# Kernel tuning notes

Measured on AMD Instinct MI355X. Metric: run time of the kernel, lower is better.

The kernel has to match this reference:

```python
import jax, jax.numpy as jnp
import numpy as np

DIM = 768
HEADS = 12
HEAD_DIM = DIM // HEADS
SCALE = HEAD_DIM ** -0.5


def setup_inputs() -> dict:
    key = jax.random.key(0)
    k1, k2, k3, k4, k5 = jax.random.split(key, 5)
    B, N = 4, 2048
    x = jax.random.normal(k1, (B, N, DIM), dtype=jnp.float32)
    # qkv Linear: weight [3*dim, dim], bias [3*dim]
    w_qkv = jax.random.normal(k2, (3 * DIM, DIM), dtype=jnp.float32) * (DIM ** -0.5)
    b_qkv = jax.random.normal(k3, (3 * DIM,), dtype=jnp.float32) * 0.01
    # proj Linear: weight [dim, dim], bias [dim]
    w_proj = jax.random.normal(k4, (DIM, DIM), dtype=jnp.float32) * (DIM ** -0.5)
    b_proj = jax.random.normal(k5, (DIM,), dtype=jnp.float32) * 0.01
    return {"x": x, "w_qkv": w_qkv, "b_qkv": b_qkv, "w_proj": w_proj, "b_proj": b_proj}


def reference(x, w_qkv, b_qkv, w_proj, b_proj):
    B, N, C = x.shape
    qkv = (jnp.einsum('bnc,oc->bno', x, w_qkv) + b_qkv)
    qkv = qkv.reshape(B, N, 3, HEADS, HEAD_DIM).transpose(2, 0, 3, 1, 4)
    q, k, v = qkv[0], qkv[1], qkv[2]
    attn = jnp.einsum('bhqd,bhkd->bhqk', q, k) * SCALE
    attn = jax.nn.softmax(attn, axis=-1)
    out = jnp.einsum('bhqk,bhkd->bhqd', attn, v)  # [B, H, N, Dh]
    out = out.transpose(0, 2, 1, 3).reshape(B, N, C)
    # dropout is identity in eval mode
    return jnp.einsum('bnc,oc->bno', out, w_proj) + b_proj
```

## Files before the change

### kernel.cpp

```cpp
#include <hip/hip_runtime.h>
#include <hip/hip_bf16.h>

using bf16 = __hip_bfloat16;
typedef __bf16 bf16x8 __attribute__((ext_vector_type(8)));
typedef short short4v __attribute__((ext_vector_type(4)));
typedef short short8v __attribute__((ext_vector_type(8)));
typedef float float4v __attribute__((ext_vector_type(4)));

#define DIM   768
#define NH    12
#define HD    64
#define SEQ   2048
#define BATCH 4
#define TOK   (BATCH * SEQ)
#define SCALE_QL2E 0.18033688011112042f

#define NX  (TOK * DIM)
#define NWQ (3 * DIM * DIM)
#define NWP (DIM * DIM)

__device__ __forceinline__ short f2bf(float f) {
  union { bf16 h; short s; } u;
  u.h = __float2bfloat16(f);
  return u.s;
}

union frag8 { short4v h[2]; short8v s; bf16x8 b; };

__device__ __forceinline__ void async_copy16(const bf16* g, short* l) {
  __builtin_amdgcn_global_load_lds(
      (const __attribute__((address_space(1))) unsigned int*)g,
      (__attribute__((address_space(3))) unsigned int*)l, 16, 0, 0);
}
__device__ __forceinline__ void async_copy4(const bf16* g, short* l) {
  __builtin_amdgcn_global_load_lds(
      (const __attribute__((address_space(1))) unsigned int*)g,
      (__attribute__((address_space(3))) unsigned int*)l, 4, 0, 0);
}

#define BARRIER __builtin_amdgcn_s_barrier()
#define LGKM0 asm volatile("s_waitcnt lgkmcnt(0)" ::: "memory")
#define VW0 asm volatile("s_waitcnt vmcnt(0)" ::: "memory")
#define NOSTG (void)0
#define NOVW  (void)0

__global__ void __launch_bounds__(256)
cvt3(const float* __restrict__ a, bf16* __restrict__ oa, long na,
     const float* __restrict__ b, bf16* __restrict__ ob, long nb,
     const float* __restrict__ c, bf16* __restrict__ oc, long nc) {
  const long i = ((long)blockIdx.x * 256 + threadIdx.x) * 8;
  const float* src; bf16* dst; long off;
  if (i < na)                { src = a; dst = oa; off = i; }
  else if (i < na + nb)      { src = b; dst = ob; off = i - na; }
  else if (i < na + nb + nc) { src = c; dst = oc; off = i - na - nb; }
  else return;
  const float4v x0 = *(const float4v*)(src + off);
  const float4v x1 = *(const float4v*)(src + off + 4);
  short8v r;
  r[0] = f2bf(x0[0]); r[1] = f2bf(x0[1]); r[2] = f2bf(x0[2]); r[3] = f2bf(x0[3]);
  r[4] = f2bf(x1[0]); r[5] = f2bf(x1[1]); r[6] = f2bf(x1[2]); r[7] = f2bf(x1[3]);
  *(short8v*)(dst + off) = r;
}

__device__ __forceinline__ void gemm_mainloop(const bf16* __restrict__ A,
                                              const bf16* __restrict__ B,
                                              short* As, short* Bs,
                                              float4v acc[4][4]) {
  const int t = threadIdx.x;
  const int w = t >> 6, l = t & 63, lr = l & 15, q = l >> 4;
  const int wr = ((w >> 1) << 6), wc = ((w & 1) << 6);

  const bf16* Ag = A + (t >> 2) * DIM + (t & 3) * 8;
  const bf16* Bg = B + (t >> 2) * DIM + (t & 3) * 8;

  for (int k0 = 0; k0 < DIM; k0 += 32) {
    __syncthreads();
    async_copy16(Ag,            &As[t * 8]);
    async_copy16(Ag + 64 * DIM, &As[2048 + t * 8]);
    async_copy16(Bg,            &Bs[t * 8]);
    async_copy16(Bg + 64 * DIM, &Bs[2048 + t * 8]);
    Ag += 32; Bg += 32;
    __syncthreads();

    bf16x8 af[4], bfv[4];
#pragma unroll
    for (int i = 0; i < 4; ++i)
      af[i] = *(const bf16x8*)&As[(wr + i * 16 + lr) * 32 + q * 8];
#pragma unroll
    for (int j = 0; j < 4; ++j)
      bfv[j] = *(const bf16x8*)&Bs[(wc + j * 16 + lr) * 32 + q * 8];
#pragma unroll
    for (int i = 0; i < 4; ++i)
#pragma unroll
      for (int j = 0; j < 4; ++j)
        acc[i][j] = __builtin_amdgcn_mfma_f32_16x16x32_bf16(af[i], bfv[j],
                                                            acc[i][j], 0, 0, 0);
  }
}

#define STGP(s, p)                                                            \
  async_copy16(pa + (p) * 32,             &As[s][t * 8]);                     \
  async_copy16(pa + 64 * DIM + (p) * 32,  &As[s][2048 + t * 8]);              \
  async_copy16(pb + (p) * 32,             &Bs[s][t * 8]);                     \
  async_copy16(pb + 64 * DIM + (p) * 32,  &Bs[s][2048 + t * 8]);              \
  async_copy16(pb + 128 * DIM + (p) * 32, &Bs[s][4096 + t * 8]);              \
  async_copy16(pb + 192 * DIM + (p) * 32, &Bs[s][6144 + t * 8]);              \
  async_copy4 (pb3 + (p) * 32,            &Bs[s][8192 + t * 2]);              \
  async_copy4 (pb3 + 16 * DIM + (p) * 32, &Bs[s][8704 + t * 2])

#define PHASE(CUR, STG_, VW_) {                                               \
  bf16x8 af[4], bfv[9];                                                       \
  _Pragma("unroll") for (int mf_ = 0; mf_ < 4; ++mf_)                         \
    af[mf_] = *(const bf16x8*)&As[CUR][mf_ * 512 + arow];                     \
  _Pragma("unroll") for (int nf_ = 0; nf_ < 9; ++nf_)                         \
    bfv[nf_] = *(const bf16x8*)&Bs[CUR][nf_ * 512 + brow];                    \
  STG_; BARRIER; LGKM0;                                                       \
  __builtin_amdgcn_s_setprio(1);                                              \
  _Pragma("unroll") for (int mf_ = 0; mf_ < 4; ++mf_)                         \
  _Pragma("unroll") for (int nf_ = 0; nf_ < 9; ++nf_)                         \
    acc[mf_][nf_] = __builtin_amdgcn_mfma_f32_16x16x32_bf16(                  \
        af[mf_], bfv[nf_], acc[mf_][nf_], 0, 0, 0);                           \
  __builtin_amdgcn_s_setprio(0); VW_; BARRIER; }

__global__ void __launch_bounds__(256, 2)
gemm_qkv(const bf16* __restrict__ X, const bf16* __restrict__ W,
         const float* __restrict__ bias,
         bf16* __restrict__ qb, bf16* __restrict__ kb, bf16* __restrict__ vb) {
  __shared__ short As[2][128 * 32];
  __shared__ short Bs[2][288 * 32];
  const int t = threadIdx.x;
  const int w = t >> 6, l = t & 63, lr = l & 15, q = l >> 4;
  const int wm = w >> 1, wn = w & 1;

  const int orig = blockIdx.x;
  const int swz = (orig & 7) * 64 + (orig >> 3);
  const int tm = swz >> 3, tn = swz & 7;
  const int row0 = tm * 128, col0 = tn * 288;

  const int sr = t >> 2;
  const int scol = (((t & 3) << 3) ^ (((sr >> 1) & 3) << 3));
  const bf16* pa  = X + (size_t)(row0 + sr) * DIM + scol;
  const bf16* pb  = W + (size_t)(col0 + sr) * DIM + scol;
  const int r3 = t >> 4;
  const int c3 = ((t & 15) << 1) ^ (((r3 >> 1) & 3) << 3);
  const bf16* pb3 = W + (size_t)(col0 + 256 + r3) * DIM + c3;

  const int acol = ((q << 3) ^ (((lr >> 1) & 3) << 3));
  const int arow = (wm * 64 + lr) * 32 + acol;
  const int brow = (wn * 144 + lr) * 32 + acol;

  float4v acc[4][9] = {};

  STGP(0, 0);
  VW0; BARRIER;

#pragma unroll 1
  for (int k = 0; k < 22; k += 2) {
    PHASE(0, STGP(1, k + 1), VW0)
    PHASE(1, STGP(0, k + 2), VW0)
  }
  PHASE(0, STGP(1, 23), VW0)
  PHASE(1, NOSTG,       NOVW)

#pragma unroll
  for (int nf = 0; nf < 9; ++nf) {
    const int gn = col0 + wn * 144 + nf * 16 + lr;
    const int which = gn / DIM;
    const int cc = gn - which * DIM;
    const int hh = cc >> 6, dd = cc & 63;
    const float bv = bias[gn];
#pragma unroll
    for (int mf = 0; mf < 4; ++mf) {
      const int gm0 = row0 + wm * 64 + mf * 16 + (q << 2);
      const int b = gm0 >> 11, n0 = gm0 & 2047;
      if (which == 2) {
        short4v pv;
#pragma unroll
        for (int r = 0; r < 4; ++r) pv[r] = f2bf(acc[mf][nf][r] + bv);
        *(short4v*)&vb[((size_t)(b * NH + hh) * HD + dd) * SEQ + n0] = pv;
      } else {
        bf16* dst = (which == 0) ? qb : kb;
        const float sc = (which == 0) ? SCALE_QL2E : 1.0f;
#pragma unroll
        for (int r = 0; r < 4; ++r)
          dst[((size_t)(b * NH + hh) * SEQ + n0 + r) * HD + dd] =
              __float2bfloat16((acc[mf][nf][r] + bv) * sc);
      }
    }
  }
}

#define STG_KV(bb, k1)                                                        \
  async_copy16(Kb + (size_t)((k1) + drow) * HD + skey,       &KV[bb][t * 8]); \
  async_copy16(Kb + (size_t)((k1) + 32 + drow) * HD + skey,  &KV[bb][2048 + t * 8]); \
  async_copy16(Vb + (size_t)drow * SEQ + (k1) + skey,        &KV[bb][4096 + t * 8]); \
  async_copy16(Vb + (size_t)(32 + drow) * SEQ + (k1) + skey, &KV[bb][6144 + t * 8])

__global__ void __launch_bounds__(256, 3)
flash_attn(const bf16* __restrict__ Qp, const bf16* __restrict__ Kp,
           const bf16* __restrict__ Vtp, bf16* __restrict__ Op) {
  const int bh = blockIdx.y, qt = blockIdx.x;
  const int t = threadIdx.x, w = t >> 6, l = t & 63, lr = l & 15, q = l >> 4;
  __shared__ short KV[2][8192];

  const bf16* Qb = Qp  + (size_t)(bh * SEQ + qt * 128) * HD;
  const bf16* Kb = Kp  + (size_t)bh * SEQ * HD;
  const bf16* Vb = Vtp + (size_t)bh * HD * SEQ;

  const int drow = t >> 3;
  const int skey = (((t & 7) ^ drow) & 7) * 8;

  bf16x8 qf[2][2];
#pragma unroll
  for (int it = 0; it < 2; ++it)
#pragma unroll
    for (int kq = 0; kq < 2; ++kq)
      qf[it][kq] = *(const bf16x8*)(Qb + (size_t)(w * 32 + it * 16 + lr) * HD +
                                    kq * 32 + q * 8);

  const int key8 = (lr & 7) << 3;

  frag8 ones;
#pragma unroll
  for (int r = 0; r < 8; ++r) ones.s[r] = (short)0x3F80;

  float4v o[2][4] = {};
  float4v lacc[2] = {};

  STG_KV(0, 0);
  VW0; BARRIER;

  for (int kt = 0; kt < 32; ++kt) {
    if (kt < 31) { STG_KV((kt + 1) & 1, (kt + 1) * 64); }
    const short* Bf = KV[kt & 1];

    float4v s[4][2] = {};
    __builtin_amdgcn_s_setprio(1);
#pragma unroll
    for (int jn = 0; jn < 4; ++jn) {
      bf16x8 kf[2];
#pragma unroll
      for (int kq = 0; kq < 2; ++kq)
        kf[kq] = *(const bf16x8*)&Bf[(jn * 16 + lr) * 64 +
                                     (((kq * 32) + (q << 3)) ^ key8)];
#pragma unroll
      for (int it = 0; it < 2; ++it)
#pragma unroll
        for (int kq = 0; kq < 2; ++kq)
          s[jn][it] = __builtin_amdgcn_mfma_f32_16x16x32_bf16(kf[kq], qf[it][kq],
                                                              s[jn][it], 0, 0, 0);
    }
    __builtin_amdgcn_s_setprio(0);

    frag8 pf[2][2];
#pragma unroll
    for (int it = 0; it < 2; ++it)
#pragma unroll
      for (int c4 = 0; c4 < 2; ++c4)
#pragma unroll
        for (int r = 0; r < 4; ++r) {
          pf[c4][it].s[r]     = f2bf(__builtin_amdgcn_exp2f(s[2 * c4][it][r]));
          pf[c4][it].s[4 + r] = f2bf(__builtin_amdgcn_exp2f(s[2 * c4 + 1][it][r]));
        }

    __builtin_amdgcn_s_setprio(1);
#pragma unroll
    for (int c4 = 0; c4 < 2; ++c4) {
#pragma unroll
      for (int dj = 0; dj < 4; ++dj) {
        frag8 vf;
        vf.h[0] = *(const short4v*)&Bf[4096 + (dj * 16 + lr) * 64 +
                                       ((c4 * 32 + (q << 2)) ^ key8)];
        vf.h[1] = *(const short4v*)&Bf[4096 + (dj * 16 + lr) * 64 +
                                       ((c4 * 32 + 16 + (q << 2)) ^ key8)];
#pragma unroll
        for (int it = 0; it < 2; ++it)
          o[it][dj] = __builtin_amdgcn_mfma_f32_16x16x32_bf16(pf[c4][it].b, vf.b,
                                                              o[it][dj], 0, 0, 0);
      }
#pragma unroll
      for (int it = 0; it < 2; ++it)
        lacc[it] = __builtin_amdgcn_mfma_f32_16x16x32_bf16(pf[c4][it].b, ones.b,
                                                           lacc[it], 0, 0, 0);
    }
    __builtin_amdgcn_s_setprio(0);

    if (kt < 31) { VW0; BARRIER; }
  }

  const int b = bh / NH, h = bh - b * NH;
#pragma unroll
  for (int it = 0; it < 2; ++it)
#pragma unroll
    for (int r = 0; r < 4; ++r) {
      const float linv = 1.0f / lacc[it][r];
      const int grow = b * SEQ + qt * 128 + w * 32 + it * 16 + (q << 2) + r;
      bf16* orow = Op + (size_t)grow * DIM + h * HD;
#pragma unroll
      for (int dj = 0; dj < 4; ++dj)
        orow[dj * 16 + lr] = __float2bfloat16(o[it][dj][r] * linv);
    }
}

__global__ void __launch_bounds__(256)
gemm_proj(const bf16* __restrict__ A, const bf16* __restrict__ W,
          const float* __restrict__ bias, float* __restrict__ out) {
  __shared__ short As[128 * 32];
  __shared__ short Bs[128 * 32];
  const int t = threadIdx.x;
  const int w = t >> 6, l = t & 63, lr = l & 15, q = l >> 4;
  const int wr = ((w >> 1) << 6), wc = ((w & 1) << 6);
  const int row0 = blockIdx.y * 128, col0 = blockIdx.x * 128;

  float4v acc[4][4] = {};
  gemm_mainloop(A + row0 * DIM, W + col0 * DIM, As, Bs, acc);

#pragma unroll
  for (int j = 0; j < 4; ++j) {
    const int gn = col0 + wc + j * 16 + lr;
    const float bv = bias[gn];
#pragma unroll
    for (int i = 0; i < 4; ++i) {
#pragma unroll
      for (int r = 0; r < 4; ++r) {
        const int gm = row0 + wr + i * 16 + (q << 2) + r;
        out[(size_t)gm * DIM + gn] = acc[i][j][r] + bv;
      }
    }
  }
}

extern "C" void kernel_launch(void* const* d_in, const int* in_sizes, int n_in,
                              void* d_out, int out_size, void* d_ws, size_t ws_size,
                              hipStream_t stream) {
  const float* x      = (const float*)d_in[0];
  const float* w_qkv  = (const float*)d_in[1];
  const float* b_qkv  = (const float*)d_in[2];
  const float* w_proj = (const float*)d_in[3];
  const float* b_proj = (const float*)d_in[4];
  float* out = (float*)d_out;

  const size_t perbuf = (size_t)BATCH * NH * SEQ * HD;
  bf16* qb  = (bf16*)d_ws;
  bf16* kb  = qb + perbuf;
  bf16* vb  = kb + perbuf;
  bf16* ao  = vb + perbuf;
  bf16* xb  = ao + perbuf;
  bf16* wqb = xb + (size_t)NX;
  bf16* wpb = wqb + (size_t)NWQ;

  const int cvt_blocks = (NX + NWQ + NWP) / 8 / 256;
  cvt3<<<cvt_blocks, 256, 0, stream>>>(x, xb, NX, w_qkv, wqb, NWQ, w_proj, wpb, NWP);
  gemm_qkv <<<dim3(512), 256, 0, stream>>>(xb, wqb, b_qkv, qb, kb, vb);
  flash_attn<<<dim3(SEQ / 128, BATCH * NH), 256, 0, stream>>>(qb, kb, vb, ao);
  gemm_proj <<<dim3(DIM / 128, TOK / 128),  256, 0, stream>>>(ao, wpb, b_proj, out);
}
```

Baseline: 202.6 us.

## Software-pipeline flash attention: overlap QK^T of next tile with PV of previous

Restructures the attention inner loop into a skewed software pipeline: each iteration computes S for tile k, then runs PV for tile k-1 using the previously exponentiated probabilities, issues the async load for tile k+1, and then exponentiates tile k. LDS grows to triple buffering so that K/V for three tiles can be live at once, and the loop is unrolled by two with ping-pong probability register fragments. The intent is to let exp2/convert work overlap with MFMA work and hide load latency. The cost is more registers and LDS, which may reduce occupancy at the requested 3 blocks per CU.

```diff
diff --git a/kernel.cpp b/kernel.cpp
--- a/kernel.cpp
+++ b/kernel.cpp
@@ -25,7 +25,7 @@
   return u.s;
 }
 
-union frag8 { short4v h[2]; short8v s; bf16x8 b; };
+union frag8 { short4v h[2]; short8v s; bf16x8 b; unsigned u[4]; };
 
 __device__ __forceinline__ void async_copy16(const bf16* g, short* l) {
   __builtin_amdgcn_global_load_lds(
@@ -196,12 +196,63 @@
   async_copy16(Vb + (size_t)drow * SEQ + (k1) + skey,        &KV[bb][4096 + t * 8]); \
   async_copy16(Vb + (size_t)(32 + drow) * SEQ + (k1) + skey, &KV[bb][6144 + t * 8])
 
+#define S_STEP(BK_) {                                                         \
+  const short* Bf_ = KV[BK_];                                                 \
+  __builtin_amdgcn_s_setprio(1);                                              \
+  _Pragma("unroll") for (int jn = 0; jn < 4; ++jn) {                          \
+    bf16x8 kf[2];                                                             \
+    _Pragma("unroll") for (int kq = 0; kq < 2; ++kq)                          \
+      kf[kq] = *(const bf16x8*)&Bf_[(jn * 16 + lr) * 64 +                     \
+                                    (((kq * 32) + (q << 3)) ^ key8)];         \
+    _Pragma("unroll") for (int it = 0; it < 2; ++it)                          \
+    _Pragma("unroll") for (int kq = 0; kq < 2; ++kq)                          \
+      s[jn][it] = __builtin_amdgcn_mfma_f32_16x16x32_bf16(kf[kq],             \
+                      qf[it][kq], s[jn][it], 0, 0, 0);                        \
+  }                                                                           \
+  __builtin_amdgcn_s_setprio(0); }
+
+#define PV_STEP(PF_, BP_) {                                                   \
+  const short* Bv_ = KV[BP_] + 4096;                                          \
+  __builtin_amdgcn_s_setprio(1);                                              \
+  _Pragma("unroll") for (int c4 = 0; c4 < 2; ++c4) {                          \
+    _Pragma("unroll") for (int dj = 0; dj < 4; ++dj) {                        \
+      frag8 vf;                                                               \
+      vf.h[0] = *(const short4v*)&Bv_[(dj * 16 + lr) * 64 +                   \
+                                      ((c4 * 32 + (q << 2)) ^ key8)];         \
+      vf.h[1] = *(const short4v*)&Bv_[(dj * 16 + lr) * 64 +                   \
+                                      ((c4 * 32 + 16 + (q << 2)) ^ key8)];    \
+      _Pragma("unroll") for (int it = 0; it < 2; ++it)                        \
+        o[it][dj] = __builtin_amdgcn_mfma_f32_16x16x32_bf16(PF_[c4][it].b,    \
+                        vf.b, o[it][dj], 0, 0, 0);                            \
+    }                                                                         \
+    _Pragma("unroll") for (int it = 0; it < 2; ++it)                          \
+      lacc[it] = __builtin_amdgcn_mfma_f32_16x16x32_bf16(PF_[c4][it].b,       \
+                     ones.b, lacc[it], 0, 0, 0);                              \
+  }                                                                           \
+  __builtin_amdgcn_s_setprio(0); }
+
+#define SM_STEP(PF_)                                                          \
+  _Pragma("unroll") for (int it = 0; it < 2; ++it)                            \
+  _Pragma("unroll") for (int c4 = 0; c4 < 2; ++c4)                            \
+  _Pragma("unroll") for (int r = 0; r < 4; ++r) {                             \
+    PF_[c4][it].s[r]     = f2bf(__builtin_amdgcn_exp2f(s[2 * c4][it][r]));    \
+    PF_[c4][it].s[4 + r] = f2bf(__builtin_amdgcn_exp2f(s[2 * c4 + 1][it][r]));\
+  }
+
+#define FA_BODY(BK_, BP_, BN_, PFP_, PFC_, TILE1_) {                          \
+  float4v s[4][2] = {};                                                       \
+  S_STEP(BK_);                                                                \
+  PV_STEP(PFP_, BP_);                                                         \
+  STG_KV(BN_, (TILE1_) * 64);                                                 \
+  SM_STEP(PFC_);                                                              \
+  VW0; BARRIER; }
+
 __global__ void __launch_bounds__(256, 3)
 flash_attn(const bf16* __restrict__ Qp, const bf16* __restrict__ Kp,
            const bf16* __restrict__ Vtp, bf16* __restrict__ Op) {
   const int bh = blockIdx.y, qt = blockIdx.x;
   const int t = threadIdx.x, w = t >> 6, l = t & 63, lr = l & 15, q = l >> 4;
-  __shared__ short KV[2][8192];
+  __shared__ short KV[3][8192];
 
   const bf16* Qb = Qp  + (size_t)(bh * SEQ + qt * 128) * HD;
   const bf16* Kb = Kp  + (size_t)bh * SEQ * HD;
@@ -226,66 +277,35 @@
 
   float4v o[2][4] = {};
   float4v lacc[2] = {};
+  frag8 pfA[2][2], pfB[2][2];
 
   STG_KV(0, 0);
   VW0; BARRIER;
 
-  for (int kt = 0; kt < 32; ++kt) {
-    if (kt < 31) { STG_KV((kt + 1) & 1, (kt + 1) * 64); }
-    const short* Bf = KV[kt & 1];
-
+  {
     float4v s[4][2] = {};
-    __builtin_amdgcn_s_setprio(1);
-#pragma unroll
-    for (int jn = 0; jn < 4; ++jn) {
-      bf16x8 kf[2];
-#pragma unroll
-      for (int kq = 0; kq < 2; ++kq)
-        kf[kq] = *(const bf16x8*)&Bf[(jn * 16 + lr) * 64 +
-                                     (((kq * 32) + (q << 3)) ^ key8)];
-#pragma unroll
-      for (int it = 0; it < 2; ++it)
-#pragma unroll
-        for (int kq = 0; kq < 2; ++kq)
-          s[jn][it] = __builtin_amdgcn_mfma_f32_16x16x32_bf16(kf[kq], qf[it][kq],
-                                                              s[jn][it], 0, 0, 0);
-    }
-    __builtin_amdgcn_s_setprio(0);
-
-    frag8 pf[2][2];
-#pragma unroll
-    for (int it = 0; it < 2; ++it)
-#pragma unroll
-      for (int c4 = 0; c4 < 2; ++c4)
-#pragma unroll
-        for (int r = 0; r < 4; ++r) {
-          pf[c4][it].s[r]     = f2bf(__builtin_amdgcn_exp2f(s[2 * c4][it][r]));
-          pf[c4][it].s[4 + r] = f2bf(__builtin_amdgcn_exp2f(s[2 * c4 + 1][it][r]));
-        }
-
-    __builtin_amdgcn_s_setprio(1);
-#pragma unroll
-    for (int c4 = 0; c4 < 2; ++c4) {
-#pragma unroll
-      for (int dj = 0; dj < 4; ++dj) {
-        frag8 vf;
-        vf.h[0] = *(const short4v*)&Bf[4096 + (dj * 16 + lr) * 64 +
-                                       ((c4 * 32 + (q << 2)) ^ key8)];
-        vf.h[1] = *(const short4v*)&Bf[4096 + (dj * 16 + lr) * 64 +
-                                       ((c4 * 32 + 16 + (q << 2)) ^ key8)];
-#pragma unroll
-        for (int it = 0; it < 2; ++it)
-          o[it][dj] = __builtin_amdgcn_mfma_f32_16x16x32_bf16(pf[c4][it].b, vf.b,
-                                                              o[it][dj], 0, 0, 0);
-      }
-#pragma unroll
-      for (int it = 0; it < 2; ++it)
-        lacc[it] = __builtin_amdgcn_mfma_f32_16x16x32_bf16(pf[c4][it].b, ones.b,
-                                                           lacc[it], 0, 0, 0);
-    }
-    __builtin_amdgcn_s_setprio(0);
-
-    if (kt < 31) { VW0; BARRIER; }
+    S_STEP(0);
+    STG_KV(1, 64);
+    SM_STEP(pfA);
+    VW0; BARRIER;
+  }
+
+  int bK = 1;
+#pragma unroll 1
+  for (int kt = 1; kt < 31; kt += 2) {
+    const int bP = (bK == 0) ? 2 : bK - 1;
+    const int bN = (bK == 2) ? 0 : bK + 1;
+    FA_BODY(bK, bP, bN, pfA, pfB, kt + 1)
+    FA_BODY(bN, bK, bP, pfB, pfA, kt + 2)
+    bK = bP;
+  }
+
+  {
+    float4v s[4][2] = {};
+    S_STEP(1);
+    PV_STEP(pfA, 0);
+    SM_STEP(pfB);
+    PV_STEP(pfB, 1);
   }
 
   const int b = bh / NH, h = bh - b * NH;
```

Measured after the change: 203.2 us. About the same (+0.3%).
